# Optimization experiments

Measured on AMD Instinct MI355X. Metric: run time of the kernel, lower is better.

## Reference

```python
import jax, jax.numpy as jnp
import numpy as np

CHUNK = 2048  # query points processed per step; bounds peak memory at [CHUNK, F, 3]


def _safe_div(num, den):
    den_s = jnp.where(jnp.abs(den) > 1e-12, den, 1.0)
    return num / den_s


def _closest_point_on_triangle(p, a, b, c):
    """Ericson's region-based closest point on triangle.
    p: [n,1,3], a/b/c: [1,F,3] -> returns [n,F,3]."""
    ab = b - a
    ac = c - a
    ap = p - a
    d1 = jnp.sum(ab * ap, -1)
    d2 = jnp.sum(ac * ap, -1)
    bp = p - b
    d3 = jnp.sum(ab * bp, -1)
    d4 = jnp.sum(ac * bp, -1)
    cpv = p - c
    d5 = jnp.sum(ab * cpv, -1)
    d6 = jnp.sum(ac * cpv, -1)
    vc = d1 * d4 - d3 * d2
    vb = d5 * d2 - d1 * d6
    va = d3 * d6 - d5 * d4
    v_ab = jnp.clip(_safe_div(d1, d1 - d3), 0.0, 1.0)
    w_ac = jnp.clip(_safe_div(d2, d2 - d6), 0.0, 1.0)
    w_bc = jnp.clip(_safe_div(d4 - d3, (d4 - d3) + (d5 - d6)), 0.0, 1.0)
    denom = va + vb + vc
    v = _safe_div(vb, denom)
    w = _safe_div(vc, denom)
    res = a + ab * v[..., None] + ac * w[..., None]  # face interior
    m_bc = (va <= 0) & ((d4 - d3) >= 0) & ((d5 - d6) >= 0)
    m_ac = (vb <= 0) & (d2 >= 0) & (d6 <= 0)
    m_ab = (vc <= 0) & (d1 >= 0) & (d3 <= 0)
    m_c = (d6 >= 0) & (d5 <= d6)
    m_b = (d3 >= 0) & (d4 <= d3)
    m_a = (d1 <= 0) & (d2 <= 0)
    res = jnp.where(m_bc[..., None], b + w_bc[..., None] * (c - b), res)
    res = jnp.where(m_ac[..., None], a + w_ac[..., None] * ac, res)
    res = jnp.where(m_ab[..., None], a + v_ab[..., None] * ab, res)
    res = jnp.where(m_c[..., None], c, res)
    res = jnp.where(m_b[..., None], b, res)
    res = jnp.where(m_a[..., None], a, res)
    return res


def _query_one_batch(tris, pts):
    # tris: [F,3,3], pts: [Q,3]
    a, b, c = tris[:, 0], tris[:, 1], tris[:, 2]

    def chunk_fn(pc):  # pc: [CHUNK,3]
        cp = _closest_point_on_triangle(pc[:, None, :], a[None], b[None], c[None])  # [CHUNK,F,3]
        d2 = jnp.sum((pc[:, None, :] - cp) ** 2, -1)  # [CHUNK,F] squared distances
        dist = jnp.min(d2, axis=-1)
        idx = jnp.argmin(d2, axis=-1)
        closest = jnp.take_along_axis(cp, idx[:, None, None], axis=1)[:, 0]
        return dist, closest, idx.astype(jnp.int32)

    Q = pts.shape[0]
    pts_c = pts.reshape(Q // CHUNK, CHUNK, 3)
    dist, closest, idx = jax.lax.map(chunk_fn, pts_c)
    return dist.reshape(Q), closest.reshape(Q, 3), idx.reshape(Q)


def setup_inputs() -> dict:
    key = jax.random.key(0)
    k1, k2 = jax.random.split(key)
    triangles = jax.random.normal(k1, (2, 4096, 3, 3), dtype=jnp.float32)
    points = jax.random.normal(k2, (2, 16384, 3), dtype=jnp.float32)
    return {"triangles": triangles, "points": points}


def reference(triangles, points):
    # distances are SQUARED point-to-mesh distances, matching the CUDA kernel
    distances, closest_points, closest_faces = jax.vmap(_query_one_batch)(triangles, points)
    return distances, closest_points, closest_faces
```

## Files before the change

### kernel.cpp

```cpp
#include <hip/hip_runtime.h>
#include <math.h>

namespace {

typedef float v2f __attribute__((ext_vector_type(2)));

constexpr int B = 2;
constexpr int F = 4096;
constexpr int Q = 16384;
constexpr int NP = B * Q;
constexpr int BLOCK = 256;
constexpr int P4 = 4;

constexpr int OFF_DIST = 0;
constexpr int OFF_CP = NP;
constexpr int OFF_FACE = 4 * NP;


__device__ __forceinline__ float safediv(float num, float den) {
  #pragma clang fp contract(off)
  float d = (fabsf(den) > 1e-12f) ? den : 1.0f;
  return num / d;
}

__device__ __forceinline__ float clamp01(float x) {
  return fminf(fmaxf(x, 0.0f), 1.0f);
}

__device__ __forceinline__ void closest_pt(
    float px, float py, float pz,
    float ax, float ay, float az,
    float bx, float by, float bz,
    float cx, float cy, float cz,
    float& rx, float& ry, float& rz) {
  #pragma clang fp contract(off)
  float abx = bx - ax, aby = by - ay, abz = bz - az;
  float acx = cx - ax, acy = cy - ay, acz = cz - az;
  float apx = px - ax, apy = py - ay, apz = pz - az;
  float d1 = (abx * apx + aby * apy) + abz * apz;
  float d2 = (acx * apx + acy * apy) + acz * apz;
  float bpx = px - bx, bpy = py - by, bpz = pz - bz;
  float d3 = (abx * bpx + aby * bpy) + abz * bpz;
  float d4 = (acx * bpx + acy * bpy) + acz * bpz;
  float cpx = px - cx, cpy = py - cy, cpz = pz - cz;
  float d5 = (abx * cpx + aby * cpy) + abz * cpz;
  float d6 = (acx * cpx + acy * cpy) + acz * cpz;

  float vc = d1 * d4 - d3 * d2;
  float vb = d5 * d2 - d1 * d6;
  float va = d3 * d6 - d5 * d4;

  float v_ab = clamp01(safediv(d1, d1 - d3));
  float w_ac = clamp01(safediv(d2, d2 - d6));
  float w_bc = clamp01(safediv(d4 - d3, (d4 - d3) + (d5 - d6)));

  float denom = (va + vb) + vc;
  float v = safediv(vb, denom);
  float w = safediv(vc, denom);

  float ox = ax + abx * v + acx * w;
  float oy = ay + aby * v + acy * w;
  float oz = az + abz * v + acz * w;

  bool m_bc = (va <= 0.0f) && (d4 - d3 >= 0.0f) && (d5 - d6 >= 0.0f);
  bool m_ac = (vb <= 0.0f) && (d2 >= 0.0f) && (d6 <= 0.0f);
  bool m_ab = (vc <= 0.0f) && (d1 >= 0.0f) && (d3 <= 0.0f);
  bool m_c  = (d6 >= 0.0f) && (d5 <= d6);
  bool m_b  = (d3 >= 0.0f) && (d4 <= d3);
  bool m_a  = (d1 <= 0.0f) && (d2 <= 0.0f);

  if (m_bc) { ox = bx + w_bc * (cx - bx); oy = by + w_bc * (cy - by); oz = bz + w_bc * (cz - bz); }
  if (m_ac) { ox = ax + w_ac * acx;       oy = ay + w_ac * acy;       oz = az + w_ac * acz; }
  if (m_ab) { ox = ax + v_ab * abx;       oy = ay + v_ab * aby;       oz = az + v_ab * abz; }
  if (m_c)  { ox = cx; oy = cy; oz = cz; }
  if (m_b)  { ox = bx; oy = by; oz = bz; }
  if (m_a)  { ox = ax; oy = ay; oz = az; }

  rx = ox; ry = oy; rz = oz;
}

__device__ __forceinline__ float exact_d2(
    float px, float py, float pz, const float* __restrict__ g ) {
  #pragma clang fp contract(off)
  float rx, ry, rz;
  closest_pt(px, py, pz,
             g[0], g[1], g[2], g[3], g[4], g[5], g[6], g[7], g[8],
             rx, ry, rz);
  float dx = px - rx, dy = py - ry, dz = pz - rz;
  return (dx * dx + dy * dy) + dz * dz;
}


__device__ __forceinline__ unsigned umin2(unsigned a, unsigned b) { return a < b ? a : b; }
__device__ __forceinline__ unsigned umax2(unsigned a, unsigned b) { return a > b ? a : b; }

__device__ __forceinline__ void ins2(unsigned k, unsigned& K1, unsigned& K2) {
  unsigned t = umax2(K1, k);
  K1 = umin2(K1, k);
  K2 = umin2(K2, t);
}

__device__ __forceinline__ void ins8(unsigned k,
    unsigned& K1, unsigned& K2, unsigned& K3, unsigned& K4,
    unsigned& K5, unsigned& K6, unsigned& K7, unsigned& K8) {
  unsigned t;
  t = umax2(K1, k); K1 = umin2(K1, k);
  k = t; t = umax2(K2, k); K2 = umin2(K2, k);
  k = t; t = umax2(K3, k); K3 = umin2(K3, k);
  k = t; t = umax2(K4, k); K4 = umin2(K4, k);
  k = t; t = umax2(K5, k); K5 = umin2(K5, k);
  k = t; t = umax2(K6, k); K6 = umin2(K6, k);
  k = t; t = umax2(K7, k); K7 = umin2(K7, k);
  K8 = umin2(K8, t);
}

__device__ __forceinline__ unsigned fin_one(
    float dint, float tabm, float tacm, float tbcm,
    float td1, float td2, float ap2m, float bp2, float t43d,
    float va, float vb, float vc,
    float aa, float bb, float cc, float pp, int gidx) {
  float tab = __builtin_amdgcn_fmed3f(tabm, 0.0f, 1.0f);
  float sab = fmaf(-tab, fmaf(-tab, aa, td1), ap2m);
  float tac = __builtin_amdgcn_fmed3f(tacm, 0.0f, 1.0f);
  float sac = fmaf(-tac, fmaf(-tac, bb, td2), ap2m);
  float tbc = __builtin_amdgcn_fmed3f(tbcm, 0.0f, 1.0f);
  float sbc = fmaf(-tbc, fmaf(-tbc, cc, t43d), bp2);
  float dseg = fminf(fminf(sab, sac), sbc);
  float mv   = fminf(fminf(va, vb), vc);
  float d = (mv > 0.0f) ? dint : dseg;
  d = fmaxf(d + pp, 0.0f);
  return (__float_as_uint(d) & 0xFFFFF000u) | (unsigned)gidx;
}


__global__ __launch_bounds__(BLOCK) void bvh_prep(
    const float* __restrict__ tris, float4* __restrict__ rec) {
  int i = blockIdx.x * BLOCK + threadIdx.x;
  if (i >= B * F) return;
  const float* g = tris + (size_t)i * 9;
  float ax = g[0], ay = g[1], az = g[2];
  float abx = g[3] - ax, aby = g[4] - ay, abz = g[5] - az;
  float acx = g[6] - ax, acy = g[7] - ay, acz = g[8] - az;
  float aa   = abx * abx + aby * aby + abz * abz;
  float bb   = acx * acx + acy * acy + acz * acz;
  float abac = abx * acx + aby * acy + abz * acz;
  float bcx = acx - abx, bcy = acy - aby, bcz = acz - abz;
  float cc   = bcx * bcx + bcy * bcy + bcz * bcz;
  float nx = aby * acz - abz * acy;
  float ny = abz * acx - abx * acz;
  float nz = abx * acy - aby * acx;
  float n2 = nx * nx + ny * ny + nz * nz;
  float raa = (aa > 1e-12f) ? 1.0f / aa : 1.0f;
  float rbb = (bb > 1e-12f) ? 1.0f / bb : 1.0f;
  float rcc = (cc > 1e-12f) ? 1.0f / cc : 1.0f;
  float rdn = (n2 > 1e-12f) ? 1.0f / n2 : 1.0f;
  float c1 = -(ax * abx + ay * aby + az * abz);
  float c2 = -(ax * acx + ay * acy + az * acz);
  float caa2 = ax * ax + ay * ay + az * az;
  float4* r = rec + (size_t)i * 5;
  r[0] = make_float4(abx, aby, abz, c1);
  r[1] = make_float4(acx, acy, acz, c2);
  r[2] = make_float4(-2.0f * ax, -2.0f * ay, -2.0f * az, caa2);
  r[3] = make_float4(aa, bb, abac, cc);
  r[4] = make_float4(raa, rbb, rcc, rdn);
}


template <int NC>
__global__ __launch_bounds__(BLOCK, 4) void bvh_screen_smem(
    const float* __restrict__ pts,
    const float4* __restrict__ rec,
    uint2* __restrict__ keys) {
  constexpr int CFL = F / NC;
  constexpr int BPB = (Q / P4) / BLOCK;
  const int batch = blockIdx.x / BPB;
  const int j = (blockIdx.x % BPB) * BLOCK + threadIdx.x;
  const int chunk = blockIdx.y;
  const int tri0 = chunk * CFL;
  const float4* rb = rec + ((size_t)batch * F + tri0) * 5;

  const int p0 = batch * Q + j;
  float px0 = pts[(p0          ) * 3 + 0], py0 = pts[(p0          ) * 3 + 1], pz0 = pts[(p0          ) * 3 + 2];
  float px1 = pts[(p0 + Q/4    ) * 3 + 0], py1 = pts[(p0 + Q/4    ) * 3 + 1], pz1 = pts[(p0 + Q/4    ) * 3 + 2];
  float px2 = pts[(p0 + Q/2    ) * 3 + 0], py2 = pts[(p0 + Q/2    ) * 3 + 1], pz2 = pts[(p0 + Q/2    ) * 3 + 2];
  float px3 = pts[(p0 + 3*(Q/4)) * 3 + 0], py3 = pts[(p0 + 3*(Q/4)) * 3 + 1], pz3 = pts[(p0 + 3*(Q/4)) * 3 + 2];

  const v2f pxA = {px0, px1}, pyA = {py0, py1}, pzA = {pz0, pz1};
  const v2f pxB = {px2, px3}, pyB = {py2, py3}, pzB = {pz2, pz3};
  const float pp0 = px0*px0 + py0*py0 + pz0*pz0;
  const float pp1 = px1*px1 + py1*py1 + pz1*pz1;
  const float pp2 = px2*px2 + py2*py2 + pz2*pz2;
  const float pp3 = px3*px3 + py3*py3 + pz3*pz3;

  unsigned A1 = ~0u, A2 = ~0u, Bk1 = ~0u, Bk2 = ~0u;
  unsigned C1 = ~0u, C2 = ~0u, D1 = ~0u, D2 = ~0u;

  {
    #pragma clang fp contract(fast)
    #pragma unroll 2
    for (int t = 0; t < CFL; ++t) {
      const float4 R0 = rb[t * 5 + 0];
      const float4 R1 = rb[t * 5 + 1];
      const float4 R2 = rb[t * 5 + 2];
      const float4 R3 = rb[t * 5 + 3];
      const float4 R4 = rb[t * 5 + 4];
      const int gidx = tri0 + t;

      {
        v2f d1   = pxA * R0.x + pyA * R0.y + pzA * R0.z + R0.w;
        v2f d2   = pxA * R1.x + pyA * R1.y + pzA * R1.z + R1.w;
        v2f ap2m = pxA * R2.x + pyA * R2.y + pzA * R2.z + R2.w;
        v2f d3 = d1 - R3.x, d6 = d2 - R3.y, d4 = d2 - R3.z, d5 = d1 - R3.z;
        v2f t43 = d4 - d3;
        v2f va = d3 * d6 - d5 * d4;
        v2f vb = d5 * d2 - d1 * d6;
        v2f vc = d1 * d4 - d3 * d2;
        v2f td1 = d1 + d1, td2 = d2 + d2;
        v2f v = vb * R4.w, w = vc * R4.w;
        v2f h1 = v * R3.x + (w * R3.z - td1);
        v2f h2 = w * R3.y + (v * R3.z - td2);
        v2f dint = ap2m + (v * h1 + w * h2);
        v2f tabm = d1 * R4.x, tacm = d2 * R4.y, tbcm = t43 * R4.z;
        v2f bp2 = (ap2m - td1) + R3.x;
        v2f t43d = t43 + t43;
        ins2(fin_one(dint.x, tabm.x, tacm.x, tbcm.x, td1.x, td2.x, ap2m.x,
                     bp2.x, t43d.x, va.x, vb.x, vc.x,
                     R3.x, R3.y, R3.w, pp0, gidx), A1, A2);
        ins2(fin_one(dint.y, tabm.y, tacm.y, tbcm.y, td1.y, td2.y, ap2m.y,
                     bp2.y, t43d.y, va.y, vb.y, vc.y,
                     R3.x, R3.y, R3.w, pp1, gidx), Bk1, Bk2);
      }
      {
        v2f d1   = pxB * R0.x + pyB * R0.y + pzB * R0.z + R0.w;
        v2f d2   = pxB * R1.x + pyB * R1.y + pzB * R1.z + R1.w;
        v2f ap2m = pxB * R2.x + pyB * R2.y + pzB * R2.z + R2.w;
        v2f d3 = d1 - R3.x, d6 = d2 - R3.y, d4 = d2 - R3.z, d5 = d1 - R3.z;
        v2f t43 = d4 - d3;
        v2f va = d3 * d6 - d5 * d4;
        v2f vb = d5 * d2 - d1 * d6;
        v2f vc = d1 * d4 - d3 * d2;
        v2f td1 = d1 + d1, td2 = d2 + d2;
        v2f v = vb * R4.w, w = vc * R4.w;
        v2f h1 = v * R3.x + (w * R3.z - td1);
        v2f h2 = w * R3.y + (v * R3.z - td2);
        v2f dint = ap2m + (v * h1 + w * h2);
        v2f tabm = d1 * R4.x, tacm = d2 * R4.y, tbcm = t43 * R4.z;
        v2f bp2 = (ap2m - td1) + R3.x;
        v2f t43d = t43 + t43;
        ins2(fin_one(dint.x, tabm.x, tacm.x, tbcm.x, td1.x, td2.x, ap2m.x,
                     bp2.x, t43d.x, va.x, vb.x, vc.x,
                     R3.x, R3.y, R3.w, pp2, gidx), C1, C2);
        ins2(fin_one(dint.y, tabm.y, tacm.y, tbcm.y, td1.y, td2.y, ap2m.y,
                     bp2.y, t43d.y, va.y, vb.y, vc.y,
                     R3.x, R3.y, R3.w, pp3, gidx), D1, D2);
      }
    }
  }

  keys[(size_t)chunk * NP + p0            ] = make_uint2(A1, A2);
  keys[(size_t)chunk * NP + p0 + Q/4      ] = make_uint2(Bk1, Bk2);
  keys[(size_t)chunk * NP + p0 + Q/2      ] = make_uint2(C1, C2);
  keys[(size_t)chunk * NP + p0 + 3*(Q/4)  ] = make_uint2(D1, D2);
}


template <int NC>
__global__ __launch_bounds__(BLOCK) void bvh_finish2(
    const float* __restrict__ tris,
    const float* __restrict__ pts,
    const uint2* __restrict__ keys,
    float* __restrict__ out) {
  const int gpt = blockIdx.x * BLOCK + threadIdx.x;
  if (gpt >= NP) return;

  unsigned K1 = ~0u, K2 = ~0u, K3 = ~0u, K4 = ~0u;
  unsigned K5 = ~0u, K6 = ~0u, K7 = ~0u, K8 = ~0u;
  for (int c = 0; c < NC; ++c) {
    uint2 k = keys[(size_t)c * NP + gpt];
    ins8(k.x, K1, K2, K3, K4, K5, K6, K7, K8);
    ins8(k.y, K1, K2, K3, K4, K5, K6, K7, K8);
  }

  const int batch = gpt / Q;
  const float* tb = tris + (size_t)batch * F * 9;
  const float px = pts[gpt * 3 + 0];
  const float py = pts[gpt * 3 + 1];
  const float pz = pts[gpt * 3 + 2];

  float be = INFINITY;
  int bi = 0x7FFFFFFF;
  #define CAND(Kx) { int t_ = (int)(Kx & 0xFFFu); \
    float d_ = exact_d2(px, py, pz, tb + (size_t)t_ * 9); \
    if (d_ < be || (d_ == be && t_ < bi)) { be = d_; bi = t_; } }
  CAND(K1) CAND(K2) CAND(K3) CAND(K4) CAND(K5) CAND(K6) CAND(K7) CAND(K8)
  #undef CAND

  const float* tr = tb + (size_t)bi * 9;
  float rx, ry, rz;
  closest_pt(px, py, pz,
             tr[0], tr[1], tr[2], tr[3], tr[4], tr[5], tr[6], tr[7], tr[8],
             rx, ry, rz);

  out[OFF_DIST + gpt] = be;
  out[OFF_CP + gpt * 3 + 0] = rx;
  out[OFF_CP + gpt * 3 + 1] = ry;
  out[OFF_CP + gpt * 3 + 2] = rz;
  out[OFF_FACE + gpt] = (float)bi;
}


template <int NC>
__global__ __launch_bounds__(BLOCK, 4) void bvh_screen4(
    const float* __restrict__ tris,
    const float* __restrict__ pts,
    uint2* __restrict__ keys) {
  constexpr int CFL = F / NC;
  __shared__ float4 s_rec[5 * CFL];

  constexpr int BPB = (Q / P4) / BLOCK;
  const int batch = blockIdx.x / BPB;
  const int j = (blockIdx.x % BPB) * BLOCK + threadIdx.x;
  const int chunk = blockIdx.y;
  const int tri0 = chunk * CFL;
  const float* tb = tris + (size_t)batch * F * 9;

  for (int t = threadIdx.x; t < CFL; t += BLOCK) {
    const float* g = tb + (size_t)(tri0 + t) * 9;
    float ax = g[0], ay = g[1], az = g[2];
    float abx = g[3] - ax, aby = g[4] - ay, abz = g[5] - az;
    float acx = g[6] - ax, acy = g[7] - ay, acz = g[8] - az;
    float aa   = abx * abx + aby * aby + abz * abz;
    float bb   = acx * acx + acy * acy + acz * acz;
    float abac = abx * acx + aby * acy + abz * acz;
    float bcx = acx - abx, bcy = acy - aby, bcz = acz - abz;
    float cc   = bcx * bcx + bcy * bcy + bcz * bcz;
    float nx = aby * acz - abz * acy;
    float ny = abz * acx - abx * acz;
    float nz = abx * acy - aby * acx;
    float n2 = nx * nx + ny * ny + nz * nz;
    float raa = (aa > 1e-12f) ? 1.0f / aa : 1.0f;
    float rbb = (bb > 1e-12f) ? 1.0f / bb : 1.0f;
    float rcc = (cc > 1e-12f) ? 1.0f / cc : 1.0f;
    float rdn = (n2 > 1e-12f) ? 1.0f / n2 : 1.0f;
    float c1 = -(ax * abx + ay * aby + az * abz);
    float c2 = -(ax * acx + ay * acy + az * acz);
    float caa2 = ax * ax + ay * ay + az * az;
    s_rec[0 * CFL + t] = make_float4(abx, aby, abz, c1);
    s_rec[1 * CFL + t] = make_float4(acx, acy, acz, c2);
    s_rec[2 * CFL + t] = make_float4(-2.0f * ax, -2.0f * ay, -2.0f * az, caa2);
    s_rec[3 * CFL + t] = make_float4(aa, bb, abac, cc);
    s_rec[4 * CFL + t] = make_float4(raa, rbb, rcc, rdn);
  }
  __syncthreads();

  const int p0 = batch * Q + j;
  float px0 = pts[(p0          ) * 3 + 0], py0 = pts[(p0          ) * 3 + 1], pz0 = pts[(p0          ) * 3 + 2];
  float px1 = pts[(p0 + Q/4    ) * 3 + 0], py1 = pts[(p0 + Q/4    ) * 3 + 1], pz1 = pts[(p0 + Q/4    ) * 3 + 2];
  float px2 = pts[(p0 + Q/2    ) * 3 + 0], py2 = pts[(p0 + Q/2    ) * 3 + 1], pz2 = pts[(p0 + Q/2    ) * 3 + 2];
  float px3 = pts[(p0 + 3*(Q/4)) * 3 + 0], py3 = pts[(p0 + 3*(Q/4)) * 3 + 1], pz3 = pts[(p0 + 3*(Q/4)) * 3 + 2];

  const v2f pxA = {px0, px1}, pyA = {py0, py1}, pzA = {pz0, pz1};
  const v2f pxB = {px2, px3}, pyB = {py2, py3}, pzB = {pz2, pz3};
  const float pp0 = px0*px0 + py0*py0 + pz0*pz0;
  const float pp1 = px1*px1 + py1*py1 + pz1*pz1;
  const float pp2 = px2*px2 + py2*py2 + pz2*pz2;
  const float pp3 = px3*px3 + py3*py3 + pz3*pz3;

  unsigned A1 = ~0u, A2 = ~0u, Bk1 = ~0u, Bk2 = ~0u;
  unsigned C1 = ~0u, C2 = ~0u, D1 = ~0u, D2 = ~0u;

  {
    #pragma clang fp contract(fast)
    for (int t = 0; t < CFL; ++t) {
      const float4 R0 = s_rec[0 * CFL + t];
      const float4 R1 = s_rec[1 * CFL + t];
      const float4 R2 = s_rec[2 * CFL + t];
      const float4 R3 = s_rec[3 * CFL + t];
      const float4 R4 = s_rec[4 * CFL + t];
      const int gidx = tri0 + t;
      {
        v2f d1   = pxA * R0.x + pyA * R0.y + pzA * R0.z + R0.w;
        v2f d2   = pxA * R1.x + pyA * R1.y + pzA * R1.z + R1.w;
        v2f ap2m = pxA * R2.x + pyA * R2.y + pzA * R2.z + R2.w;
        v2f d3 = d1 - R3.x, d6 = d2 - R3.y, d4 = d2 - R3.z, d5 = d1 - R3.z;
        v2f t43 = d4 - d3;
        v2f va = d3 * d6 - d5 * d4;
        v2f vb = d5 * d2 - d1 * d6;
        v2f vc = d1 * d4 - d3 * d2;
        v2f td1 = d1 + d1, td2 = d2 + d2;
        v2f v = vb * R4.w, w = vc * R4.w;
        v2f h1 = v * R3.x + (w * R3.z - td1);
        v2f h2 = w * R3.y + (v * R3.z - td2);
        v2f dint = ap2m + (v * h1 + w * h2);
        v2f tabm = d1 * R4.x, tacm = d2 * R4.y, tbcm = t43 * R4.z;
        v2f bp2 = (ap2m - td1) + R3.x;
        v2f t43d = t43 + t43;
        ins2(fin_one(dint.x, tabm.x, tacm.x, tbcm.x, td1.x, td2.x, ap2m.x,
                     bp2.x, t43d.x, va.x, vb.x, vc.x,
                     R3.x, R3.y, R3.w, pp0, gidx), A1, A2);
        ins2(fin_one(dint.y, tabm.y, tacm.y, tbcm.y, td1.y, td2.y, ap2m.y,
                     bp2.y, t43d.y, va.y, vb.y, vc.y,
                     R3.x, R3.y, R3.w, pp1, gidx), Bk1, Bk2);
      }
      {
        v2f d1   = pxB * R0.x + pyB * R0.y + pzB * R0.z + R0.w;
        v2f d2   = pxB * R1.x + pyB * R1.y + pzB * R1.z + R1.w;
        v2f ap2m = pxB * R2.x + pyB * R2.y + pzB * R2.z + R2.w;
        v2f d3 = d1 - R3.x, d6 = d2 - R3.y, d4 = d2 - R3.z, d5 = d1 - R3.z;
        v2f t43 = d4 - d3;
        v2f va = d3 * d6 - d5 * d4;
        v2f vb = d5 * d2 - d1 * d6;
        v2f vc = d1 * d4 - d3 * d2;
        v2f td1 = d1 + d1, td2 = d2 + d2;
        v2f v = vb * R4.w, w = vc * R4.w;
        v2f h1 = v * R3.x + (w * R3.z - td1);
        v2f h2 = w * R3.y + (v * R3.z - td2);
        v2f dint = ap2m + (v * h1 + w * h2);
        v2f tabm = d1 * R4.x, tacm = d2 * R4.y, tbcm = t43 * R4.z;
        v2f bp2 = (ap2m - td1) + R3.x;
        v2f t43d = t43 + t43;
        ins2(fin_one(dint.x, tabm.x, tacm.x, tbcm.x, td1.x, td2.x, ap2m.x,
                     bp2.x, t43d.x, va.x, vb.x, vc.x,
                     R3.x, R3.y, R3.w, pp2, gidx), C1, C2);
        ins2(fin_one(dint.y, tabm.y, tacm.y, tbcm.y, td1.y, td2.y, ap2m.y,
                     bp2.y, t43d.y, va.y, vb.y, vc.y,
                     R3.x, R3.y, R3.w, pp3, gidx), D1, D2);
      }
    }
  }

  keys[(size_t)chunk * NP + p0            ] = make_uint2(A1, A2);
  keys[(size_t)chunk * NP + p0 + Q/4      ] = make_uint2(Bk1, Bk2);
  keys[(size_t)chunk * NP + p0 + Q/2      ] = make_uint2(C1, C2);
  keys[(size_t)chunk * NP + p0 + 3*(Q/4)  ] = make_uint2(D1, D2);
}

}

extern "C" void kernel_launch(void* const* d_in, const int* in_sizes, int n_in,
                              void* d_out, int out_size, void* d_ws, size_t ws_size,
                              hipStream_t stream) {
  const float* tris = (const float*)d_in[0];
  const float* pts  = (const float*)d_in[1];
  float* out = (float*)d_out;

  dim3 grid2((NP + BLOCK - 1) / BLOCK);

  constexpr int NC = 32;
  constexpr size_t KEY_BYTES = (size_t)NC * NP * sizeof(uint2);
  constexpr size_t REC_BYTES = (size_t)B * F * 5 * sizeof(float4);
  const int gx = B * ((Q / P4) / BLOCK);

  if (ws_size >= KEY_BYTES + REC_BYTES) {
    uint2* keys = (uint2*)d_ws;
    float4* rec = (float4*)((char*)d_ws + KEY_BYTES);
    bvh_prep<<<(B * F + BLOCK - 1) / BLOCK, BLOCK, 0, stream>>>(tris, rec);
    bvh_screen_smem<NC><<<dim3(gx, NC), BLOCK, 0, stream>>>(pts, rec, keys);
    bvh_finish2<NC><<<grid2, BLOCK, 0, stream>>>(tris, pts, keys, out);
  } else {
    uint2* keys = (uint2*)d_ws;
    bvh_screen4<NC><<<dim3(gx, NC), BLOCK, 0, stream>>>(tris, pts, keys);
    bvh_finish2<NC><<<grid2, BLOCK, 0, stream>>>(tris, pts, keys, out);
  }
}
```

Before: 172.1 us.

## Drop global prep pass; use shared-memory screen with 64 chunks and higher occupancy

Removes the separate triangle preprocessing kernel and the global-record screen kernel. The default path now uses the shared-memory screen kernel, which builds per-triangle records in LDS itself, with 64 face chunks and launch bounds requesting 8 waves per EU. This removes one launch and the global record traffic, and doubles the grid to improve occupancy. In exchange the finish kernel must merge twice as many candidate key pairs, and the tighter register budget may cause spills.

```diff
diff --git a/kernel.cpp b/kernel.cpp
--- a/kernel.cpp
+++ b/kernel.cpp
@@ -133,184 +133,8 @@
 }
 
 
-__global__ __launch_bounds__(BLOCK) void bvh_prep(
-    const float* __restrict__ tris, float4* __restrict__ rec) {
-  int i = blockIdx.x * BLOCK + threadIdx.x;
-  if (i >= B * F) return;
-  const float* g = tris + (size_t)i * 9;
-  float ax = g[0], ay = g[1], az = g[2];
-  float abx = g[3] - ax, aby = g[4] - ay, abz = g[5] - az;
-  float acx = g[6] - ax, acy = g[7] - ay, acz = g[8] - az;
-  float aa   = abx * abx + aby * aby + abz * abz;
-  float bb   = acx * acx + acy * acy + acz * acz;
-  float abac = abx * acx + aby * acy + abz * acz;
-  float bcx = acx - abx, bcy = acy - aby, bcz = acz - abz;
-  float cc   = bcx * bcx + bcy * bcy + bcz * bcz;
-  float nx = aby * acz - abz * acy;
-  float ny = abz * acx - abx * acz;
-  float nz = abx * acy - aby * acx;
-  float n2 = nx * nx + ny * ny + nz * nz;
-  float raa = (aa > 1e-12f) ? 1.0f / aa : 1.0f;
-  float rbb = (bb > 1e-12f) ? 1.0f / bb : 1.0f;
-  float rcc = (cc > 1e-12f) ? 1.0f / cc : 1.0f;
-  float rdn = (n2 > 1e-12f) ? 1.0f / n2 : 1.0f;
-  float c1 = -(ax * abx + ay * aby + az * abz);
-  float c2 = -(ax * acx + ay * acy + az * acz);
-  float caa2 = ax * ax + ay * ay + az * az;
-  float4* r = rec + (size_t)i * 5;
-  r[0] = make_float4(abx, aby, abz, c1);
-  r[1] = make_float4(acx, acy, acz, c2);
-  r[2] = make_float4(-2.0f * ax, -2.0f * ay, -2.0f * az, caa2);
-  r[3] = make_float4(aa, bb, abac, cc);
-  r[4] = make_float4(raa, rbb, rcc, rdn);
-}
-
-
-template <int NC>
-__global__ __launch_bounds__(BLOCK, 4) void bvh_screen_smem(
-    const float* __restrict__ pts,
-    const float4* __restrict__ rec,
-    uint2* __restrict__ keys) {
-  constexpr int CFL = F / NC;
-  constexpr int BPB = (Q / P4) / BLOCK;
-  const int batch = blockIdx.x / BPB;
-  const int j = (blockIdx.x % BPB) * BLOCK + threadIdx.x;
-  const int chunk = blockIdx.y;
-  const int tri0 = chunk * CFL;
-  const float4* rb = rec + ((size_t)batch * F + tri0) * 5;
-
-  const int p0 = batch * Q + j;
-  float px0 = pts[(p0          ) * 3 + 0], py0 = pts[(p0          ) * 3 + 1], pz0 = pts[(p0          ) * 3 + 2];
-  float px1 = pts[(p0 + Q/4    ) * 3 + 0], py1 = pts[(p0 + Q/4    ) * 3 + 1], pz1 = pts[(p0 + Q/4    ) * 3 + 2];
-  float px2 = pts[(p0 + Q/2    ) * 3 + 0], py2 = pts[(p0 + Q/2    ) * 3 + 1], pz2 = pts[(p0 + Q/2    ) * 3 + 2];
-  float px3 = pts[(p0 + 3*(Q/4)) * 3 + 0], py3 = pts[(p0 + 3*(Q/4)) * 3 + 1], pz3 = pts[(p0 + 3*(Q/4)) * 3 + 2];
-
-  const v2f pxA = {px0, px1}, pyA = {py0, py1}, pzA = {pz0, pz1};
-  const v2f pxB = {px2, px3}, pyB = {py2, py3}, pzB = {pz2, pz3};
-  const float pp0 = px0*px0 + py0*py0 + pz0*pz0;
-  const float pp1 = px1*px1 + py1*py1 + pz1*pz1;
-  const float pp2 = px2*px2 + py2*py2 + pz2*pz2;
-  const float pp3 = px3*px3 + py3*py3 + pz3*pz3;
-
-  unsigned A1 = ~0u, A2 = ~0u, Bk1 = ~0u, Bk2 = ~0u;
-  unsigned C1 = ~0u, C2 = ~0u, D1 = ~0u, D2 = ~0u;
-
-  {
-    #pragma clang fp contract(fast)
-    #pragma unroll 2
-    for (int t = 0; t < CFL; ++t) {
-      const float4 R0 = rb[t * 5 + 0];
-      const float4 R1 = rb[t * 5 + 1];
-      const float4 R2 = rb[t * 5 + 2];
-      const float4 R3 = rb[t * 5 + 3];
-      const float4 R4 = rb[t * 5 + 4];
-      const int gidx = tri0 + t;
-
-      {
-        v2f d1   = pxA * R0.x + pyA * R0.y + pzA * R0.z + R0.w;
-        v2f d2   = pxA * R1.x + pyA * R1.y + pzA * R1.z + R1.w;
-        v2f ap2m = pxA * R2.x + pyA * R2.y + pzA * R2.z + R2.w;
-        v2f d3 = d1 - R3.x, d6 = d2 - R3.y, d4 = d2 - R3.z, d5 = d1 - R3.z;
-        v2f t43 = d4 - d3;
-        v2f va = d3 * d6 - d5 * d4;
-        v2f vb = d5 * d2 - d1 * d6;
-        v2f vc = d1 * d4 - d3 * d2;
-        v2f td1 = d1 + d1, td2 = d2 + d2;
-        v2f v = vb * R4.w, w = vc * R4.w;
-        v2f h1 = v * R3.x + (w * R3.z - td1);
-        v2f h2 = w * R3.y + (v * R3.z - td2);
-        v2f dint = ap2m + (v * h1 + w * h2);
-        v2f tabm = d1 * R4.x, tacm = d2 * R4.y, tbcm = t43 * R4.z;
-        v2f bp2 = (ap2m - td1) + R3.x;
-        v2f t43d = t43 + t43;
-        ins2(fin_one(dint.x, tabm.x, tacm.x, tbcm.x, td1.x, td2.x, ap2m.x,
-                     bp2.x, t43d.x, va.x, vb.x, vc.x,
-                     R3.x, R3.y, R3.w, pp0, gidx), A1, A2);
-        ins2(fin_one(dint.y, tabm.y, tacm.y, tbcm.y, td1.y, td2.y, ap2m.y,
-                     bp2.y, t43d.y, va.y, vb.y, vc.y,
-                     R3.x, R3.y, R3.w, pp1, gidx), Bk1, Bk2);
-      }
-      {
-        v2f d1   = pxB * R0.x + pyB * R0.y + pzB * R0.z + R0.w;
-        v2f d2   = pxB * R1.x + pyB * R1.y + pzB * R1.z + R1.w;
-        v2f ap2m = pxB * R2.x + pyB * R2.y + pzB * R2.z + R2.w;
-        v2f d3 = d1 - R3.x, d6 = d2 - R3.y, d4 = d2 - R3.z, d5 = d1 - R3.z;
-        v2f t43 = d4 - d3;
-        v2f va = d3 * d6 - d5 * d4;
-        v2f vb = d5 * d2 - d1 * d6;
-        v2f vc = d1 * d4 - d3 * d2;
-        v2f td1 = d1 + d1, td2 = d2 + d2;
-        v2f v = vb * R4.w, w = vc * R4.w;
-        v2f h1 = v * R3.x + (w * R3.z - td1);
-        v2f h2 = w * R3.y + (v * R3.z - td2);
-        v2f dint = ap2m + (v * h1 + w * h2);
-        v2f tabm = d1 * R4.x, tacm = d2 * R4.y, tbcm = t43 * R4.z;
-        v2f bp2 = (ap2m - td1) + R3.x;
-        v2f t43d = t43 + t43;
-        ins2(fin_one(dint.x, tabm.x, tacm.x, tbcm.x, td1.x, td2.x, ap2m.x,
-                     bp2.x, t43d.x, va.x, vb.x, vc.x,
-                     R3.x, R3.y, R3.w, pp2, gidx), C1, C2);
-        ins2(fin_one(dint.y, tabm.y, tacm.y, tbcm.y, td1.y, td2.y, ap2m.y,
-                     bp2.y, t43d.y, va.y, vb.y, vc.y,
-                     R3.x, R3.y, R3.w, pp3, gidx), D1, D2);
-      }
-    }
-  }
-
-  keys[(size_t)chunk * NP + p0            ] = make_uint2(A1, A2);
-  keys[(size_t)chunk * NP + p0 + Q/4      ] = make_uint2(Bk1, Bk2);
-  keys[(size_t)chunk * NP + p0 + Q/2      ] = make_uint2(C1, C2);
-  keys[(size_t)chunk * NP + p0 + 3*(Q/4)  ] = make_uint2(D1, D2);
-}
-
-
-template <int NC>
-__global__ __launch_bounds__(BLOCK) void bvh_finish2(
-    const float* __restrict__ tris,
-    const float* __restrict__ pts,
-    const uint2* __restrict__ keys,
-    float* __restrict__ out) {
-  const int gpt = blockIdx.x * BLOCK + threadIdx.x;
-  if (gpt >= NP) return;
-
-  unsigned K1 = ~0u, K2 = ~0u, K3 = ~0u, K4 = ~0u;
-  unsigned K5 = ~0u, K6 = ~0u, K7 = ~0u, K8 = ~0u;
-  for (int c = 0; c < NC; ++c) {
-    uint2 k = keys[(size_t)c * NP + gpt];
-    ins8(k.x, K1, K2, K3, K4, K5, K6, K7, K8);
-    ins8(k.y, K1, K2, K3, K4, K5, K6, K7, K8);
-  }
-
-  const int batch = gpt / Q;
-  const float* tb = tris + (size_t)batch * F * 9;
-  const float px = pts[gpt * 3 + 0];
-  const float py = pts[gpt * 3 + 1];
-  const float pz = pts[gpt * 3 + 2];
-
-  float be = INFINITY;
-  int bi = 0x7FFFFFFF;
-  #define CAND(Kx) { int t_ = (int)(Kx & 0xFFFu); \
-    float d_ = exact_d2(px, py, pz, tb + (size_t)t_ * 9); \
-    if (d_ < be || (d_ == be && t_ < bi)) { be = d_; bi = t_; } }
-  CAND(K1) CAND(K2) CAND(K3) CAND(K4) CAND(K5) CAND(K6) CAND(K7) CAND(K8)
-  #undef CAND
-
-  const float* tr = tb + (size_t)bi * 9;
-  float rx, ry, rz;
-  closest_pt(px, py, pz,
-             tr[0], tr[1], tr[2], tr[3], tr[4], tr[5], tr[6], tr[7], tr[8],
-             rx, ry, rz);
-
-  out[OFF_DIST + gpt] = be;
-  out[OFF_CP + gpt * 3 + 0] = rx;
-  out[OFF_CP + gpt * 3 + 1] = ry;
-  out[OFF_CP + gpt * 3 + 2] = rz;
-  out[OFF_FACE + gpt] = (float)bi;
-}
-
-
-template <int NC>
-__global__ __launch_bounds__(BLOCK, 4) void bvh_screen4(
+template <int NC, int WPE>
+__global__ __launch_bounds__(BLOCK, WPE) void bvh_screen4(
     const float* __restrict__ tris,
     const float* __restrict__ pts,
     uint2* __restrict__ keys) {
@@ -435,6 +259,51 @@
   keys[(size_t)chunk * NP + p0 + 3*(Q/4)  ] = make_uint2(D1, D2);
 }
 
+
+template <int NC>
+__global__ __launch_bounds__(BLOCK) void bvh_finish2(
+    const float* __restrict__ tris,
+    const float* __restrict__ pts,
+    const uint2* __restrict__ keys,
+    float* __restrict__ out) {
+  const int gpt = blockIdx.x * BLOCK + threadIdx.x;
+  if (gpt >= NP) return;
+
+  unsigned K1 = ~0u, K2 = ~0u, K3 = ~0u, K4 = ~0u;
+  unsigned K5 = ~0u, K6 = ~0u, K7 = ~0u, K8 = ~0u;
+  for (int c = 0; c < NC; ++c) {
+    uint2 k = keys[(size_t)c * NP + gpt];
+    ins8(k.x, K1, K2, K3, K4, K5, K6, K7, K8);
+    ins8(k.y, K1, K2, K3, K4, K5, K6, K7, K8);
+  }
+
+  const int batch = gpt / Q;
+  const float* tb = tris + (size_t)batch * F * 9;
+  const float px = pts[gpt * 3 + 0];
+  const float py = pts[gpt * 3 + 1];
+  const float pz = pts[gpt * 3 + 2];
+
+  float be = INFINITY;
+  int bi = 0x7FFFFFFF;
+  #define CAND(Kx) { int t_ = (int)(Kx & 0xFFFu); \
+    float d_ = exact_d2(px, py, pz, tb + (size_t)t_ * 9); \
+    if (d_ < be || (d_ == be && t_ < bi)) { be = d_; bi = t_; } }
+  CAND(K1) CAND(K2) CAND(K3) CAND(K4) CAND(K5) CAND(K6) CAND(K7) CAND(K8)
+  #undef CAND
+
+  const float* tr = tb + (size_t)bi * 9;
+  float rx, ry, rz;
+  closest_pt(px, py, pz,
+             tr[0], tr[1], tr[2], tr[3], tr[4], tr[5], tr[6], tr[7], tr[8],
+             rx, ry, rz);
+
+  out[OFF_DIST + gpt] = be;
+  out[OFF_CP + gpt * 3 + 0] = rx;
+  out[OFF_CP + gpt * 3 + 1] = ry;
+  out[OFF_CP + gpt * 3 + 2] = rz;
+  out[OFF_FACE + gpt] = (float)bi;
+}
+
 }
 
 extern "C" void kernel_launch(void* const* d_in, const int* in_sizes, int n_in,
@@ -445,21 +314,18 @@
   float* out = (float*)d_out;
 
   dim3 grid2((NP + BLOCK - 1) / BLOCK);
-
-  constexpr int NC = 32;
-  constexpr size_t KEY_BYTES = (size_t)NC * NP * sizeof(uint2);
-  constexpr size_t REC_BYTES = (size_t)B * F * 5 * sizeof(float4);
   const int gx = B * ((Q / P4) / BLOCK);
 
-  if (ws_size >= KEY_BYTES + REC_BYTES) {
+  constexpr size_t KEY64_BYTES = (size_t)64 * NP * sizeof(uint2);
+  constexpr size_t KEY32_BYTES = (size_t)32 * NP * sizeof(uint2);
+
+  if (ws_size >= KEY64_BYTES) {
     uint2* keys = (uint2*)d_ws;
-    float4* rec = (float4*)((char*)d_ws + KEY_BYTES);
-    bvh_prep<<<(B * F + BLOCK - 1) / BLOCK, BLOCK, 0, stream>>>(tris, rec);
-    bvh_screen_smem<NC><<<dim3(gx, NC), BLOCK, 0, stream>>>(pts, rec, keys);
-    bvh_finish2<NC><<<grid2, BLOCK, 0, stream>>>(tris, pts, keys, out);
+    bvh_screen4<64, 8><<<dim3(gx, 64), BLOCK, 0, stream>>>(tris, pts, keys);
+    bvh_finish2<64><<<grid2, BLOCK, 0, stream>>>(tris, pts, keys, out);
   } else {
     uint2* keys = (uint2*)d_ws;
-    bvh_screen4<NC><<<dim3(gx, NC), BLOCK, 0, stream>>>(tris, pts, keys);
-    bvh_finish2<NC><<<grid2, BLOCK, 0, stream>>>(tris, pts, keys, out);
+    bvh_screen4<32, 4><<<dim3(gx, 32), BLOCK, 0, stream>>>(tris, pts, keys);
+    bvh_finish2<32><<<grid2, BLOCK, 0, stream>>>(tris, pts, keys, out);
   }
 }
```

Result: slower. 224.4 us (+30.4%).
